# Kernel optimization log

Hardware: AMD Instinct MI355X
Metric: run time of the kernel (lower is better)

Reference implementation:

```python
import jax, jax.numpy as jnp
import numpy as np

N_NODES = 100000
N_EDGES = 1600000
D = 128


def _gine_layer(x, src, dst, e, W1, b1, W2, b2):
    # message: relu(x_j + e_ji), aggregate: sum at destination
    m = jax.nn.relu(x[src] + e)                       # [E, D]
    agg = jax.ops.segment_sum(m, dst, num_segments=x.shape[0])  # [N, D]
    h = agg + x                                       # (1 + eps) * x_i with eps = 0
    h = jax.nn.relu(jnp.dot(h, W1) + b1)
    return jnp.dot(h, W2) + b2


def setup_inputs() -> dict:
    key = jax.random.key(0)
    ks = jax.random.split(key, 16)
    s = 0.05
    inp = {
        "x": jax.random.normal(ks[0], (N_NODES, D), dtype=jnp.float32),
        "edge_index": jax.random.randint(ks[1], (2, N_EDGES), 0, N_NODES, dtype=jnp.int64) if jax.config.jax_enable_x64 else jax.random.randint(ks[1], (2, N_EDGES), 0, N_NODES, dtype=jnp.int32),
        "edge_attr": jax.random.randint(ks[2], (N_EDGES,), 0, 100, dtype=jnp.int32),
        "edge_emb": jax.random.normal(ks[3], (100, D), dtype=jnp.float32) * s,
        "Win": jax.random.normal(ks[4], (D, D), dtype=jnp.float32) * s,
        "b_in": jnp.zeros((D,), dtype=jnp.float32),
        "W1_0": jax.random.normal(ks[5], (D, D), dtype=jnp.float32) * s,
        "b1_0": jnp.zeros((D,), dtype=jnp.float32),
        "W2_0": jax.random.normal(ks[6], (D, D), dtype=jnp.float32) * s,
        "b2_0": jnp.zeros((D,), dtype=jnp.float32),
        "W1_1": jax.random.normal(ks[7], (D, D), dtype=jnp.float32) * s,
        "b1_1": jnp.zeros((D,), dtype=jnp.float32),
        "W2_1": jax.random.normal(ks[8], (D, D), dtype=jnp.float32) * s,
        "b2_1": jnp.zeros((D,), dtype=jnp.float32),
        "Wout": jax.random.normal(ks[9], (D, 1), dtype=jnp.float32) * s,
        "b_out": jnp.zeros((1,), dtype=jnp.float32),
    }
    return inp


def reference(x, edge_index, edge_attr, edge_emb, Win, b_in,
              W1_0, b1_0, W2_0, b2_0, W1_1, b1_1, W2_1, b2_1,
              Wout, b_out):
    src, dst = edge_index[0], edge_index[1]
    e = edge_emb[edge_attr]                 # [E, D] edge-attribute embedding lookup
    h = jnp.dot(x, Win) + b_in              # input_proj
    # layer 0: GINEConv + residual add + relu (norm=none, dropout off)
    h = jax.nn.relu(_gine_layer(h, src, dst, e, W1_0, b1_0, W2_0, b2_0) + h)
    # layer 1
    h = jax.nn.relu(_gine_layer(h, src, dst, e, W1_1, b1_1, W2_1, b2_1) + h)
    # output_mlp: single Linear(hidden, 1); no final activation, no pooling
    return jnp.dot(h, Wout) + b_out
```

## Files before the change

kernel.cpp:

```cpp
#include <hip/hip_runtime.h>

#define NN 100000
#define D 128
#define CHUNK 4096
#define BCSTRIDE 392

typedef __attribute__((ext_vector_type(8))) short short8;
typedef __attribute__((ext_vector_type(8))) unsigned short ushort8;
typedef __attribute__((ext_vector_type(4))) float f32x4;

__device__ __forceinline__ float4 ld4(const float* p) { return *(const float4*)p; }

__device__ __forceinline__ unsigned short f2bf(float f) {
    unsigned int u = __float_as_uint(f);
    unsigned int r = u + 0x7fffu + ((u >> 16) & 1u);
    return (unsigned short)(r >> 16);
}
__device__ __forceinline__ float bf2f(unsigned short h) {
    return __uint_as_float(((unsigned int)h) << 16);
}
__device__ __forceinline__ float blo(unsigned int u) { return __uint_as_float(u << 16); }
__device__ __forceinline__ float bhi(unsigned int u) { return __uint_as_float(u & 0xffff0000u); }

__device__ __forceinline__ int swz(int r, int c) {
    return r * 128 + ((((c >> 2) ^ (r & 7)) << 2) | (c & 3));
}
__device__ __forceinline__ int pidx(int p, int r, int c) {
    return p * 8192 + r * 128 + (((c >> 3) ^ (r & 7)) << 3) + (c & 7);
}

__device__ __forceinline__ void coop_gemm8(
    const unsigned short* Hs,
    const unsigned short* __restrict__ Whi, const unsigned short* __restrict__ Wlo,
    int wv, int lane, int lr, int q, f32x4 acc[4])
{
    #pragma unroll
    for (int ks = 0; ks < 4; ++ks) {
        short8 ahi[4], alo[4];
        #pragma unroll
        for (int m = 0; m < 4; ++m) {
            const int row = m * 16 + lr;
            const int c   = ks * 32 + q * 8;
            ahi[m] = *(const short8*)&Hs[pidx(0, row, c)];
            alo[m] = *(const short8*)&Hs[pidx(1, row, c)];
        }
        const int base = ((wv * 4 + ks) * 64 + lane) * 8;
        const short8 bhi8 = *(const short8*)&Whi[base];
        const short8 blo8 = *(const short8*)&Wlo[base];
        #pragma unroll
        for (int m = 0; m < 4; ++m) {
            acc[m] = __builtin_amdgcn_mfma_f32_16x16x32_bf16(alo[m], bhi8, acc[m], 0, 0, 0);
            acc[m] = __builtin_amdgcn_mfma_f32_16x16x32_bf16(ahi[m], blo8, acc[m], 0, 0, 0);
            acc[m] = __builtin_amdgcn_mfma_f32_16x16x32_bf16(ahi[m], bhi8, acc[m], 0, 0, 0);
        }
    }
}

__device__ __forceinline__ void gemm_in_body(
    unsigned short* Hs, int bid,
    const float* __restrict__ A1,
    const unsigned short* __restrict__ Whi, const unsigned short* __restrict__ Wlo,
    const float* __restrict__ bias,
    unsigned short* __restrict__ out_hi, unsigned short* __restrict__ out_lo, int N)
{
    const int t    = threadIdx.x;
    const int wv   = t >> 6;
    const int lane = t & 63;
    const int lr   = lane & 15;
    const int q    = lane >> 4;
    const int rE   = wv * 8 + (lane >> 3);
    const int cE   = (lane & 7) * 16;
    const int rowE = bid * 64 + rE;

    {
        float v[16];
        if (rowE < N) {
            const int off = rowE * D + cE;
            #pragma unroll
            for (int k = 0; k < 4; ++k) {
                const float4 x = ld4(&A1[off + k * 4]);
                v[k * 4 + 0] = x.x; v[k * 4 + 1] = x.y; v[k * 4 + 2] = x.z; v[k * 4 + 3] = x.w;
            }
        } else {
            #pragma unroll
            for (int j = 0; j < 16; ++j) v[j] = 0.f;
        }
        #pragma unroll
        for (int h8 = 0; h8 < 2; ++h8) {
            ushort8 hv, lv;
            #pragma unroll
            for (int j = 0; j < 8; ++j) {
                const float f = v[h8 * 8 + j];
                const unsigned short hi = f2bf(f);
                hv[j] = hi;
                lv[j] = f2bf(f - bf2f(hi));
            }
            *(ushort8*)&Hs[pidx(0, rE, cE + h8 * 8)] = hv;
            *(ushort8*)&Hs[pidx(1, rE, cE + h8 * 8)] = lv;
        }
    }
    __syncthreads();

    f32x4 acc[4];
    #pragma unroll
    for (int m = 0; m < 4; ++m) acc[m] = (f32x4){0.f, 0.f, 0.f, 0.f};
    coop_gemm8(Hs, Whi, Wlo, wv, lane, lr, q, acc);
    __syncthreads();

    unsigned int* uT = (unsigned int*)Hs;
    {
        const float b = bias[wv * 16 + lr];
        #pragma unroll
        for (int m = 0; m < 4; ++m)
            #pragma unroll
            for (int r = 0; r < 4; ++r)
                uT[swz(m * 16 + q * 4 + r, wv * 16 + lr)] = __float_as_uint(acc[m][r] + b);
    }
    __syncthreads();

    if (rowE < N) {
        const int off = rowE * D + cE;
        unsigned int w[16];
        #pragma unroll
        for (int k = 0; k < 4; ++k) {
            const uint4 a = *(const uint4*)&uT[swz(rE, cE + k * 4)];
            w[k * 4 + 0] = a.x; w[k * 4 + 1] = a.y; w[k * 4 + 2] = a.z; w[k * 4 + 3] = a.w;
        }
        #pragma unroll
        for (int h8 = 0; h8 < 2; ++h8) {
            ushort8 oh, ol;
            #pragma unroll
            for (int j = 0; j < 8; ++j) {
                const float o = __uint_as_float(w[h8 * 8 + j]);
                const unsigned short h = f2bf(o);
                oh[j] = h;
                ol[j] = f2bf(o - bf2f(h));
            }
            *(ushort8*)&out_hi[off + h8 * 8] = oh;
            *(ushort8*)&out_lo[off + h8 * 8] = ol;
        }
    }
}

__global__ __launch_bounds__(256) void setup_all(
    const float* __restrict__ W0, const float* __restrict__ W1,
    const float* __restrict__ W2, const float* __restrict__ W3,
    const float* __restrict__ W4, unsigned short* __restrict__ wp,
    const float* __restrict__ emb, unsigned int* __restrict__ embp,
    int* __restrict__ binTotal)
{
    const int T = blockIdx.x * 256 + threadIdx.x;
    if (T < 5 * D * D) {
        const int w = T / (D * D);
        const int t = T % (D * D);
        const float* W = (w == 0) ? W0 : (w == 1) ? W1 : (w == 2) ? W2 : (w == 3) ? W3 : W4;
        const int j  = t & 7;
        const int L  = (t >> 3) & 63;
        const int ks = (t >> 9) & 3;
        const int nt = t >> 11;
        const float v = W[(ks * 32 + (L >> 4) * 8 + j) * D + nt * 16 + (L & 15)];
        const unsigned short h = f2bf(v);
        unsigned short* hi = wp + (size_t)w * 2 * D * D;
        hi[t] = h;
        hi[D * D + t] = f2bf(v - bf2f(h));
    } else if (T < 5 * D * D + 6400) {
        const int i = T - 5 * D * D;
        embp[i] = (unsigned int)f2bf(emb[i * 2]) | ((unsigned int)f2bf(emb[i * 2 + 1]) << 16);
    } else if (T < 5 * D * D + 6400 + BCSTRIDE) {
        binTotal[T - 5 * D * D - 6400] = 0;
    }
}

__global__ __launch_bounds__(512, 8) void fuse_count_gemm(
    const int* __restrict__ dst, int* __restrict__ blkcnt,
    int* __restrict__ binTotal, int E, int nbins, int csrB,
    const float* __restrict__ A1,
    const unsigned short* __restrict__ Whi, const unsigned short* __restrict__ Wlo,
    const float* __restrict__ bias,
    unsigned short* __restrict__ out_hi, unsigned short* __restrict__ out_lo,
    int N, int gemmBase)
{
    __shared__ __align__(16) unsigned short Hs[2 * 64 * 128];
    if ((int)blockIdx.x < csrB) {
        int* hist = (int*)Hs;
        const int t = threadIdx.x;
        const int i = blockIdx.x;
        for (int k = t; k < nbins; k += 512) hist[k] = 0;
        __syncthreads();
        const int e0 = i * CHUNK;
        const int e1 = min(E, e0 + CHUNK);
        for (int e = e0 + t; e < e1; e += 512) atomicAdd(&hist[dst[e] >> 8], 1);
        __syncthreads();
        for (int k = t; k < nbins; k += 512) {
            const int c = hist[k];
            blkcnt[i * BCSTRIDE + k] = c;
            if (c) atomicAdd(&binTotal[k], c);
        }
    } else {
        gemm_in_body(Hs, blockIdx.x - csrB + gemmBase, A1, Whi, Wlo, bias, out_hi, out_lo, N);
    }
}

__global__ __launch_bounds__(512) void bin_scan(
    const int* __restrict__ binTotal, int* __restrict__ binStart,
    int* __restrict__ binCursor, int nbins)
{
    __shared__ int s[512];
    const int t = threadIdx.x;
    const int v = (t < nbins) ? binTotal[t] : 0;
    s[t] = v;
    __syncthreads();
    for (int off = 1; off < 512; off <<= 1) {
        const int x = (t >= off) ? s[t - off] : 0;
        __syncthreads();
        s[t] += x;
        __syncthreads();
    }
    if (t < nbins) { binStart[t] = s[t] - v; binCursor[t] = s[t] - v; }
    if (t == 0)    binStart[nbins] = s[511];
}

__global__ __launch_bounds__(512, 8) void fuse_scatter_gemm(
    const int* __restrict__ src, const int* __restrict__ dst,
    const int* __restrict__ attr, const int* __restrict__ blkcnt,
    int* __restrict__ binCursor, int2* __restrict__ binned, int E, int nbins, int csrB,
    const float* __restrict__ A1,
    const unsigned short* __restrict__ Whi, const unsigned short* __restrict__ Wlo,
    const float* __restrict__ bias,
    unsigned short* __restrict__ out_hi, unsigned short* __restrict__ out_lo,
    int N, int gemmBase)
{
    __shared__ __align__(16) unsigned short Hs[2 * 64 * 128];
    if ((int)blockIdx.x < csrB) {
        int* cur = (int*)Hs;
        const int t = threadIdx.x;
        const int i = blockIdx.x;
        for (int k = t; k < nbins; k += 512) {
            const int c = blkcnt[i * BCSTRIDE + k];
            if (c) cur[k] = atomicAdd(&binCursor[k], c);
        }
        __syncthreads();
        const int e0 = i * CHUNK;
        const int e1 = min(E, e0 + CHUNK);
        for (int e = e0 + t; e < e1; e += 512) {
            const int d = dst[e];
            const int p = atomicAdd(&cur[d >> 8], 1);
            binned[p] = make_int2(src[e] | (attr[e] << 20), d);
        }
    } else {
        gemm_in_body(Hs, blockIdx.x - csrB + gemmBase, A1, Whi, Wlo, bias, out_hi, out_lo, N);
    }
}

__global__ __launch_bounds__(512, 8) void fuse_build_gemm(
    const int2* __restrict__ binned, const int* __restrict__ binStart,
    int* __restrict__ rowptr, int* __restrict__ epack, int csrB,
    const float* __restrict__ A1,
    const unsigned short* __restrict__ Whi, const unsigned short* __restrict__ Wlo,
    const float* __restrict__ bias,
    unsigned short* __restrict__ out_hi, unsigned short* __restrict__ out_lo,
    int N, int gemmBase)
{
    __shared__ __align__(16) unsigned short Hs[2 * 64 * 128];
    if ((int)blockIdx.x < csrB) {
        int* hist = (int*)Hs;
        int* scn  = (int*)Hs + 256;
        int* curn = (int*)Hs + 512;
        const int t = threadIdx.x;
        const int b = blockIdx.x;
        if (t < 256) hist[t] = 0;
        __syncthreads();
        const int ebeg = binStart[b];
        const int eend = binStart[b + 1];
        for (int e = ebeg + t; e < eend; e += 512) atomicAdd(&hist[binned[e].y & 255], 1);
        __syncthreads();
        if (t < 256) scn[t] = hist[t];
        __syncthreads();
        for (int off = 1; off < 256; off <<= 1) {
            int x = 0;
            if (t < 256 && t >= off) x = scn[t - off];
            __syncthreads();
            if (t < 256) scn[t] += x;
            __syncthreads();
        }
        if (t < 256) {
            const int node = b * 256 + t;
            if (node < N) rowptr[node] = ebeg + scn[t];
            curn[t] = ebeg + scn[t] - hist[t];
        }
        __syncthreads();
        for (int e = ebeg + t; e < eend; e += 512) {
            const int2 v = binned[e];
            const int p = atomicAdd(&curn[v.y & 255], 1);
            epack[p] = v.x;
        }
    } else {
        gemm_in_body(Hs, blockIdx.x - csrB + gemmBase, A1, Whi, Wlo, bias, out_hi, out_lo, N);
    }
}

template<bool LAST>
__global__ __launch_bounds__(512, 8) void gine_fused(
    const unsigned short* __restrict__ h_hi, const unsigned short* __restrict__ h_lo,
    const int* __restrict__ rowptr, const int* __restrict__ epack,
    const unsigned int* __restrict__ embp,
    const unsigned short* __restrict__ W1hi, const unsigned short* __restrict__ W1lo,
    const float* __restrict__ b1,
    const unsigned short* __restrict__ W2hi, const unsigned short* __restrict__ W2lo,
    const float* __restrict__ b2,
    unsigned short* __restrict__ out_hi, unsigned short* __restrict__ out_lo,
    const float* __restrict__ Wout, const float* __restrict__ bout,
    float* __restrict__ outv, int N)
{
    __shared__ __align__(16) unsigned short Hs[2 * 64 * 128];
    const int t    = threadIdx.x;
    const int wv   = t >> 6;
    const int lane = t & 63;
    const int lr   = lane & 15;
    const int q    = lane >> 4;
    const int rE   = wv * 8 + (lane >> 3);
    const int cE   = (lane & 7) * 16;
    const int rowE = blockIdx.x * 64 + rE;

    const unsigned int* hu = (const unsigned int*)h_hi;
    const unsigned int* hl = (const unsigned int*)h_lo;

    for (int i = 0; i < 8; ++i) {
        const int row  = wv * 8 + i;
        const int node = blockIdx.x * 64 + row;
        if (node >= N) break;
        int start = (node == 0) ? 0 : rowptr[node - 1];
        int end   = rowptr[node];
        start = __builtin_amdgcn_readfirstlane(start);
        end   = __builtin_amdgcn_readfirstlane(end);

        float ax = 0.f, ay = 0.f;
        int j = start;

        for (; j < end && (j & 3); ++j) {
            const int p0 = __builtin_amdgcn_readfirstlane(epack[j]);
            const unsigned int u0 = hu[(p0 & 0xFFFFF) * 64 + lane];
            const unsigned int v0 = embp[(p0 >> 20) * 64 + lane];
            ax += fmaxf(blo(u0) + blo(v0), 0.f);
            ay += fmaxf(bhi(u0) + bhi(v0), 0.f);
        }

        for (; j + 7 < end; j += 8) {
            const int4 pk0 = *(const int4*)&epack[j];
            const int4 pk1 = *(const int4*)&epack[j + 4];
            int p[8];
            p[0] = __builtin_amdgcn_readfirstlane(pk0.x);
            p[1] = __builtin_amdgcn_readfirstlane(pk0.y);
            p[2] = __builtin_amdgcn_readfirstlane(pk0.z);
            p[3] = __builtin_amdgcn_readfirstlane(pk0.w);
            p[4] = __builtin_amdgcn_readfirstlane(pk1.x);
            p[5] = __builtin_amdgcn_readfirstlane(pk1.y);
            p[6] = __builtin_amdgcn_readfirstlane(pk1.z);
            p[7] = __builtin_amdgcn_readfirstlane(pk1.w);
            unsigned int u[8], v[8];
            #pragma unroll
            for (int k = 0; k < 8; ++k) u[k] = hu[(p[k] & 0xFFFFF) * 64 + lane];
            #pragma unroll
            for (int k = 0; k < 8; ++k) v[k] = embp[(p[k] >> 20) * 64 + lane];
            #pragma unroll
            for (int k = 0; k < 8; ++k) {
                ax += fmaxf(blo(u[k]) + blo(v[k]), 0.f);
                ay += fmaxf(bhi(u[k]) + bhi(v[k]), 0.f);
            }
        }

        if (j + 3 < end) {
            const int4 pk0 = *(const int4*)&epack[j];
            int p[4];
            p[0] = __builtin_amdgcn_readfirstlane(pk0.x);
            p[1] = __builtin_amdgcn_readfirstlane(pk0.y);
            p[2] = __builtin_amdgcn_readfirstlane(pk0.z);
            p[3] = __builtin_amdgcn_readfirstlane(pk0.w);
            unsigned int u[4], v[4];
            #pragma unroll
            for (int k = 0; k < 4; ++k) u[k] = hu[(p[k] & 0xFFFFF) * 64 + lane];
            #pragma unroll
            for (int k = 0; k < 4; ++k) v[k] = embp[(p[k] >> 20) * 64 + lane];
            #pragma unroll
            for (int k = 0; k < 4; ++k) {
                ax += fmaxf(blo(u[k]) + blo(v[k]), 0.f);
                ay += fmaxf(bhi(u[k]) + bhi(v[k]), 0.f);
            }
            j += 4;
        }

        for (; j < end; ++j) {
            const int p0 = __builtin_amdgcn_readfirstlane(epack[j]);
            const unsigned int u0 = hu[(p0 & 0xFFFFF) * 64 + lane];
            const unsigned int v0 = embp[(p0 >> 20) * 64 + lane];
            ax += fmaxf(blo(u0) + blo(v0), 0.f);
            ay += fmaxf(bhi(u0) + bhi(v0), 0.f);
        }

        const unsigned int uh = hu[node * 64 + lane];
        const unsigned int ul = hl[node * 64 + lane];
        const float vx = ax + blo(uh) + blo(ul);
        const float vy = ay + bhi(uh) + bhi(ul);
        const unsigned int hx = f2bf(vx), hy = f2bf(vy);
        const unsigned int lx = f2bf(vx - bf2f((unsigned short)hx));
        const unsigned int ly = f2bf(vy - bf2f((unsigned short)hy));
        *(unsigned int*)&Hs[pidx(0, row, 2 * lane)] = hx | (hy << 16);
        *(unsigned int*)&Hs[pidx(1, row, 2 * lane)] = lx | (ly << 16);
    }
    __syncthreads();

    f32x4 acc[4];
    #pragma unroll
    for (int m = 0; m < 4; ++m) acc[m] = (f32x4){0.f, 0.f, 0.f, 0.f};
    coop_gemm8(Hs, W1hi, W1lo, wv, lane, lr, q, acc);
    __syncthreads();

    {
        const float b = b1[wv * 16 + lr];
        const int col = wv * 16 + lr;
        #pragma unroll
        for (int m = 0; m < 4; ++m)
            #pragma unroll
            for (int r = 0; r < 4; ++r) {
                const int row = m * 16 + q * 4 + r;
                const float o = fmaxf(acc[m][r] + b, 0.f);
                const unsigned short hi = f2bf(o);
                Hs[pidx(0, row, col)] = hi;
                Hs[pidx(1, row, col)] = f2bf(o - bf2f(hi));
            }
    }
    __syncthreads();

    f32x4 acc2[4];
    #pragma unroll
    for (int m = 0; m < 4; ++m) acc2[m] = (f32x4){0.f, 0.f, 0.f, 0.f};
    coop_gemm8(Hs, W2hi, W2lo, wv, lane, lr, q, acc2);
    __syncthreads();

    unsigned int* uT = (unsigned int*)Hs;
    {
        const float b = b2[wv * 16 + lr];
        #pragma unroll
        for (int m = 0; m < 4; ++m)
            #pragma unroll
            for (int r = 0; r < 4; ++r)
                uT[swz(m * 16 + q * 4 + r, wv * 16 + lr)] = __float_as_uint(acc2[m][r] + b);
    }
    __syncthreads();

    if (LAST) {
        float accv = 0.f;
        if (rowE < N) {
            const int off = rowE * D + cE;
            unsigned int w[16];
            #pragma unroll
            for (int k = 0; k < 4; ++k) {
                const uint4 a = *(const uint4*)&uT[swz(rE, cE + k * 4)];
                w[k * 4 + 0] = a.x; w[k * 4 + 1] = a.y; w[k * 4 + 2] = a.z; w[k * 4 + 3] = a.w;
            }
            #pragma unroll
            for (int h8 = 0; h8 < 2; ++h8) {
                const ushort8 hh = *(const ushort8*)&h_hi[off + h8 * 8];
                const ushort8 ll = *(const ushort8*)&h_lo[off + h8 * 8];
                const float4 w0 = ld4(&Wout[cE + h8 * 8]);
                const float4 w1 = ld4(&Wout[cE + h8 * 8 + 4]);
                float o[8];
                #pragma unroll
                for (int j = 0; j < 8; ++j)
                    o[j] = fmaxf(__uint_as_float(w[h8 * 8 + j]) + bf2f(hh[j]) + bf2f(ll[j]), 0.f);
                accv += o[0] * w0.x + o[1] * w0.y + o[2] * w0.z + o[3] * w0.w;
                accv += o[4] * w1.x + o[5] * w1.y + o[6] * w1.z + o[7] * w1.w;
            }
        }
        accv += __shfl_xor(accv, 1);
        accv += __shfl_xor(accv, 2);
        accv += __shfl_xor(accv, 4);
        if ((lane & 7) == 0 && rowE < N) outv[rowE] = accv + bout[0];
    } else if (rowE < N) {
        const int off = rowE * D + cE;
        unsigned int w[16];
        #pragma unroll
        for (int k = 0; k < 4; ++k) {
            const uint4 a = *(const uint4*)&uT[swz(rE, cE + k * 4)];
            w[k * 4 + 0] = a.x; w[k * 4 + 1] = a.y; w[k * 4 + 2] = a.z; w[k * 4 + 3] = a.w;
        }
        #pragma unroll
        for (int h8 = 0; h8 < 2; ++h8) {
            const ushort8 hh = *(const ushort8*)&h_hi[off + h8 * 8];
            const ushort8 ll = *(const ushort8*)&h_lo[off + h8 * 8];
            ushort8 oh, ol;
            #pragma unroll
            for (int j = 0; j < 8; ++j) {
                const float o = fmaxf(__uint_as_float(w[h8 * 8 + j]) + bf2f(hh[j]) + bf2f(ll[j]), 0.f);
                const unsigned short h = f2bf(o);
                oh[j] = h;
                ol[j] = f2bf(o - bf2f(h));
            }
            *(ushort8*)&out_hi[off + h8 * 8] = oh;
            *(ushort8*)&out_lo[off + h8 * 8] = ol;
        }
    }
}

extern "C" void kernel_launch(void* const* d_in, const int* in_sizes, int n_in,
                              void* d_out, int out_size, void* d_ws, size_t ws_size,
                              hipStream_t stream)
{
    const float* x     = (const float*)d_in[0];
    const int*   ei    = (const int*)  d_in[1];
    const int*   attr  = (const int*)  d_in[2];
    const float* emb   = (const float*)d_in[3];
    const float* Win   = (const float*)d_in[4];
    const float* b_in  = (const float*)d_in[5];
    const float* W1_0  = (const float*)d_in[6];
    const float* b1_0  = (const float*)d_in[7];
    const float* W2_0  = (const float*)d_in[8];
    const float* b2_0  = (const float*)d_in[9];
    const float* W1_1  = (const float*)d_in[10];
    const float* b1_1  = (const float*)d_in[11];
    const float* W2_1  = (const float*)d_in[12];
    const float* b2_1  = (const float*)d_in[13];
    const float* Wout  = (const float*)d_in[14];
    const float* b_out = (const float*)d_in[15];
    float* out = (float*)d_out;

    const int N = NN;
    const int E = in_sizes[2];
    const int* srcp = ei;
    const int* dstp = ei + E;
    const int nbins = (N + 255) >> 8;
    const int eblocks = (E + CHUNK - 1) / CHUNK;

    unsigned short* h_hi = (unsigned short*)d_ws;
    unsigned short* h_lo = h_hi + (size_t)N * D;
    float* aggspace = (float*)(h_lo + (size_t)N * D);
    int*   rowptr = (int*)(aggspace + (size_t)N * D);
    int*   epack  = rowptr + N;
    unsigned short* wp = (unsigned short*)(epack + E);
    unsigned short* Whi[5], *Wlo[5];
    for (int i = 0; i < 5; ++i) {
        Whi[i] = wp + (size_t)i * 2 * D * D;
        Wlo[i] = Whi[i] + D * D;
    }
    unsigned int* embp = (unsigned int*)(wp + 5 * 2 * D * D);
    int2* binned    = (int2*)aggspace;
    int*  blkcnt    = (int*)(binned + E);
    int*  binTotal  = blkcnt + eblocks * BCSTRIDE;
    int*  binStart  = binTotal + BCSTRIDE;
    int*  binCursor = binStart + BCSTRIDE;
    unsigned short* hB_hi = (unsigned short*)aggspace;
    unsigned short* hB_lo = hB_hi + (size_t)N * D;

    const int fgrid = (N + 63) / 64;
    const int sgrid = (5 * D * D + 6400 + BCSTRIDE + 255) / 256;

    const int G1 = 200;
    const int G2 = 700;
    const int G3 = fgrid - G1 - G2;

    setup_all<<<sgrid, dim3(256), 0, stream>>>(Win, W1_0, W2_0, W1_1, W2_1, wp, emb, embp, binTotal);

    fuse_count_gemm<<<eblocks + G1, dim3(512), 0, stream>>>(
        dstp, blkcnt, binTotal, E, nbins, eblocks,
        x, Whi[0], Wlo[0], b_in, h_hi, h_lo, N, 0);
    bin_scan<<<1, 512, 0, stream>>>(binTotal, binStart, binCursor, nbins);
    fuse_scatter_gemm<<<eblocks + G2, dim3(512), 0, stream>>>(
        srcp, dstp, attr, blkcnt, binCursor, binned, E, nbins, eblocks,
        x, Whi[0], Wlo[0], b_in, h_hi, h_lo, N, G1);
    fuse_build_gemm<<<nbins + G3, dim3(512), 0, stream>>>(
        binned, binStart, rowptr, epack, nbins,
        x, Whi[0], Wlo[0], b_in, h_hi, h_lo, N, G1 + G2);

    gine_fused<false><<<fgrid, dim3(512), 0, stream>>>(
        h_hi, h_lo, rowptr, epack, embp,
        Whi[1], Wlo[1], b1_0, Whi[2], Wlo[2], b2_0,
        hB_hi, hB_lo, nullptr, nullptr, nullptr, N);

    gine_fused<true><<<fgrid, dim3(512), 0, stream>>>(
        hB_hi, hB_lo, rowptr, epack, embp,
        Whi[3], Wlo[3], b1_1, Whi[4], Wlo[4], b2_1,
        nullptr, nullptr, Wout, b_out, out, N);
}
```

Measured before the change: 393.3 us.

## Build CSR with per-node global atomic counts instead of two-pass binning

Replaces the three-stage binned CSR construction (bin histogram, bin scatter, per-bin local sort) with per-node global atomic counters, a per-bin node scan, and a direct scatter into the final edge array. This drops one kernel launch and the intermediate binned int2 buffer round trip. In exchange it adds 1.6M global atomics in both count and scatter phases with random addresses, and the order of edges within each node becomes nondeterministic. The input-projection GEMM blocks are redistributed across the two remaining fused kernels.

```diff
diff --git a/kernel.cpp b/kernel.cpp
--- a/kernel.cpp
+++ b/kernel.cpp
@@ -147,7 +147,7 @@
     const float* __restrict__ W2, const float* __restrict__ W3,
     const float* __restrict__ W4, unsigned short* __restrict__ wp,
     const float* __restrict__ emb, unsigned int* __restrict__ embp,
-    int* __restrict__ binTotal)
+    int* __restrict__ binTotal, int* __restrict__ ncnt, int N)
 {
     const int T = blockIdx.x * 256 + threadIdx.x;
     if (T < 5 * D * D) {
@@ -168,11 +168,13 @@
         embp[i] = (unsigned int)f2bf(emb[i * 2]) | ((unsigned int)f2bf(emb[i * 2 + 1]) << 16);
     } else if (T < 5 * D * D + 6400 + BCSTRIDE) {
         binTotal[T - 5 * D * D - 6400] = 0;
+    } else if (T < 5 * D * D + 6400 + BCSTRIDE + N) {
+        ncnt[T - 5 * D * D - 6400 - BCSTRIDE] = 0;
     }
 }
 
 __global__ __launch_bounds__(512, 8) void fuse_count_gemm(
-    const int* __restrict__ dst, int* __restrict__ blkcnt,
+    const int* __restrict__ dst, int* __restrict__ ncnt,
     int* __restrict__ binTotal, int E, int nbins, int csrB,
     const float* __restrict__ A1,
     const unsigned short* __restrict__ Whi, const unsigned short* __restrict__ Wlo,
@@ -189,11 +191,14 @@
         __syncthreads();
         const int e0 = i * CHUNK;
         const int e1 = min(E, e0 + CHUNK);
-        for (int e = e0 + t; e < e1; e += 512) atomicAdd(&hist[dst[e] >> 8], 1);
+        for (int e = e0 + t; e < e1; e += 512) {
+            const int d = dst[e];
+            atomicAdd(&ncnt[d], 1);
+            atomicAdd(&hist[d >> 8], 1);
+        }
         __syncthreads();
         for (int k = t; k < nbins; k += 512) {
             const int c = hist[k];
-            blkcnt[i * BCSTRIDE + k] = c;
             if (c) atomicAdd(&binTotal[k], c);
         }
     } else {
@@ -202,8 +207,7 @@
 }
 
 __global__ __launch_bounds__(512) void bin_scan(
-    const int* __restrict__ binTotal, int* __restrict__ binStart,
-    int* __restrict__ binCursor, int nbins)
+    const int* __restrict__ binTotal, int* __restrict__ binStart, int nbins)
 {
     __shared__ int s[512];
     const int t = threadIdx.x;
@@ -216,14 +220,38 @@
         s[t] += x;
         __syncthreads();
     }
-    if (t < nbins) { binStart[t] = s[t] - v; binCursor[t] = s[t] - v; }
+    if (t < nbins) binStart[t] = s[t] - v;
     if (t == 0)    binStart[nbins] = s[511];
+}
+
+__global__ __launch_bounds__(256) void node_scan(
+    const int* __restrict__ ncnt, const int* __restrict__ binStart,
+    int* __restrict__ rowptr, int* __restrict__ ncur, int N)
+{
+    __shared__ int scn[256];
+    const int t = threadIdx.x;
+    const int b = blockIdx.x;
+    const int node = b * 256 + t;
+    const int c = (node < N) ? ncnt[node] : 0;
+    scn[t] = c;
+    __syncthreads();
+    for (int off = 1; off < 256; off <<= 1) {
+        const int x = (t >= off) ? scn[t - off] : 0;
+        __syncthreads();
+        scn[t] += x;
+        __syncthreads();
+    }
+    if (node < N) {
+        const int end = binStart[b] + scn[t];
+        rowptr[node] = end;
+        ncur[node]   = end - c;
+    }
 }
 
 __global__ __launch_bounds__(512, 8) void fuse_scatter_gemm(
     const int* __restrict__ src, const int* __restrict__ dst,
-    const int* __restrict__ attr, const int* __restrict__ blkcnt,
-    int* __restrict__ binCursor, int2* __restrict__ binned, int E, int nbins, int csrB,
+    const int* __restrict__ attr, int* __restrict__ ncur,
+    int* __restrict__ epack, int E, int csrB,
     const float* __restrict__ A1,
     const unsigned short* __restrict__ Whi, const unsigned short* __restrict__ Wlo,
     const float* __restrict__ bias,
@@ -232,67 +260,14 @@
 {
     __shared__ __align__(16) unsigned short Hs[2 * 64 * 128];
     if ((int)blockIdx.x < csrB) {
-        int* cur = (int*)Hs;
         const int t = threadIdx.x;
         const int i = blockIdx.x;
-        for (int k = t; k < nbins; k += 512) {
-            const int c = blkcnt[i * BCSTRIDE + k];
-            if (c) cur[k] = atomicAdd(&binCursor[k], c);
-        }
-        __syncthreads();
         const int e0 = i * CHUNK;
         const int e1 = min(E, e0 + CHUNK);
         for (int e = e0 + t; e < e1; e += 512) {
             const int d = dst[e];
-            const int p = atomicAdd(&cur[d >> 8], 1);
-            binned[p] = make_int2(src[e] | (attr[e] << 20), d);
-        }
-    } else {
-        gemm_in_body(Hs, blockIdx.x - csrB + gemmBase, A1, Whi, Wlo, bias, out_hi, out_lo, N);
-    }
-}
-
-__global__ __launch_bounds__(512, 8) void fuse_build_gemm(
-    const int2* __restrict__ binned, const int* __restrict__ binStart,
-    int* __restrict__ rowptr, int* __restrict__ epack, int csrB,
-    const float* __restrict__ A1,
-    const unsigned short* __restrict__ Whi, const unsigned short* __restrict__ Wlo,
-    const float* __restrict__ bias,
-    unsigned short* __restrict__ out_hi, unsigned short* __restrict__ out_lo,
-    int N, int gemmBase)
-{
-    __shared__ __align__(16) unsigned short Hs[2 * 64 * 128];
-    if ((int)blockIdx.x < csrB) {
-        int* hist = (int*)Hs;
-        int* scn  = (int*)Hs + 256;
-        int* curn = (int*)Hs + 512;
-        const int t = threadIdx.x;
-        const int b = blockIdx.x;
-        if (t < 256) hist[t] = 0;
-        __syncthreads();
-        const int ebeg = binStart[b];
-        const int eend = binStart[b + 1];
-        for (int e = ebeg + t; e < eend; e += 512) atomicAdd(&hist[binned[e].y & 255], 1);
-        __syncthreads();
-        if (t < 256) scn[t] = hist[t];
-        __syncthreads();
-        for (int off = 1; off < 256; off <<= 1) {
-            int x = 0;
-            if (t < 256 && t >= off) x = scn[t - off];
-            __syncthreads();
-            if (t < 256) scn[t] += x;
-            __syncthreads();
-        }
-        if (t < 256) {
-            const int node = b * 256 + t;
-            if (node < N) rowptr[node] = ebeg + scn[t];
-            curn[t] = ebeg + scn[t] - hist[t];
-        }
-        __syncthreads();
-        for (int e = ebeg + t; e < eend; e += 512) {
-            const int2 v = binned[e];
-            const int p = atomicAdd(&curn[v.y & 255], 1);
-            epack[p] = v.x;
+            const int p = atomicAdd(&ncur[d], 1);
+            epack[p] = src[e] | (attr[e] << 20);
         }
     } else {
         gemm_in_body(Hs, blockIdx.x - csrB + gemmBase, A1, Whi, Wlo, bias, out_hi, out_lo, N);
@@ -543,33 +518,30 @@
         Wlo[i] = Whi[i] + D * D;
     }
     unsigned int* embp = (unsigned int*)(wp + 5 * 2 * D * D);
-    int2* binned    = (int2*)aggspace;
-    int*  blkcnt    = (int*)(binned + E);
-    int*  binTotal  = blkcnt + eblocks * BCSTRIDE;
-    int*  binStart  = binTotal + BCSTRIDE;
-    int*  binCursor = binStart + BCSTRIDE;
+    int* ncnt     = (int*)aggspace;
+    int* ncur     = ncnt + N;
+    int* binTotal = ncur + N;
+    int* binStart = binTotal + BCSTRIDE;
     unsigned short* hB_hi = (unsigned short*)aggspace;
     unsigned short* hB_lo = hB_hi + (size_t)N * D;
 
     const int fgrid = (N + 63) / 64;
-    const int sgrid = (5 * D * D + 6400 + BCSTRIDE + 255) / 256;
-
-    const int G1 = 200;
-    const int G2 = 700;
-    const int G3 = fgrid - G1 - G2;
-
-    setup_all<<<sgrid, dim3(256), 0, stream>>>(Win, W1_0, W2_0, W1_1, W2_1, wp, emb, embp, binTotal);
+    const int sgrid = (5 * D * D + 6400 + BCSTRIDE + N + 255) / 256;
+
+    const int G1 = 700;
+    const int G2 = fgrid - G1;
+
+    setup_all<<<sgrid, dim3(256), 0, stream>>>(Win, W1_0, W2_0, W1_1, W2_1, wp, emb, embp,
+                                               binTotal, ncnt, N);
 
     fuse_count_gemm<<<eblocks + G1, dim3(512), 0, stream>>>(
-        dstp, blkcnt, binTotal, E, nbins, eblocks,
+        dstp, ncnt, binTotal, E, nbins, eblocks,
         x, Whi[0], Wlo[0], b_in, h_hi, h_lo, N, 0);
-    bin_scan<<<1, 512, 0, stream>>>(binTotal, binStart, binCursor, nbins);
+    bin_scan<<<1, 512, 0, stream>>>(binTotal, binStart, nbins);
+    node_scan<<<nbins, dim3(256), 0, stream>>>(ncnt, binStart, rowptr, ncur, N);
     fuse_scatter_gemm<<<eblocks + G2, dim3(512), 0, stream>>>(
-        srcp, dstp, attr, blkcnt, binCursor, binned, E, nbins, eblocks,
+        srcp, dstp, attr, ncur, epack, E, eblocks,
         x, Whi[0], Wlo[0], b_in, h_hi, h_lo, N, G1);
-    fuse_build_gemm<<<nbins + G3, dim3(512), 0, stream>>>(
-        binned, binStart, rowptr, epack, nbins,
-        x, Whi[0], Wlo[0], b_in, h_hi, h_lo, N, G1 + G2);
 
     gine_fused<false><<<fgrid, dim3(512), 0, stream>>>(
         h_hi, h_lo, rowptr, epack, embp,
```

Result: slower. 487.0 us (+23.8%).
